# Performance work log

Measured on AMD Instinct MI355X. Metric: run time of the kernel, lower is better.

Reference implementation:

```python
import jax, jax.numpy as jnp
import numpy as np

EPS = 0.0  # torch code divides by norms directly (no eps); inputs are randn so norms > 0


def setup_inputs() -> dict:
    key = jax.random.key(0)
    ks = jax.random.split(key, 16)
    B, C, H, W = 16, 64, 128, 128
    DIM = 4 * C  # 256
    f32 = jnp.float32
    inp = {
        "low": jax.random.normal(ks[0], (B, C, H, W), f32),
        "high": jax.random.normal(ks[1], (B, C, H, W), f32),
        "flow": jax.random.normal(ks[2], (B, C, H, W), f32),
        "feedback": jax.random.normal(ks[3], (B, C, H, W), f32),
        # GCN(4, 64, 64): single graph-conv layer, relu(adj @ x @ W + b)
        "Wgcn": jax.random.normal(ks[4], (C, C), f32) * 0.05,
        "bgcn": jnp.zeros((C,), f32),
        # four SE fc heads: Linear(DIM -> C) + sigmoid
        "W1": jax.random.normal(ks[5], (C, DIM), f32) * 0.05,
        "b1": jnp.zeros((C,), f32),
        "W2": jax.random.normal(ks[6], (C, DIM), f32) * 0.05,
        "b2": jnp.zeros((C,), f32),
        "W3": jax.random.normal(ks[7], (C, DIM), f32) * 0.05,
        "b3": jnp.zeros((C,), f32),
        "W4": jax.random.normal(ks[8], (C, DIM), f32) * 0.05,
        "b4": jnp.zeros((C,), f32),
        # gate: 1x1 Conv2d(DIM -> 64) stored as dense [64, DIM]
        "Wgate": jax.random.normal(ks[9], (C, DIM), f32) * 0.05,
        "bgate": jnp.zeros((C,), f32),
    }
    return inp


def reference(low, high, flow, feedback, Wgcn, bgcn, W1, b1, W2, b2, W3, b3, W4, b4, Wgate, bgate):
    B, C, H, W = low.shape
    # adaptive avg pool(1) of concat([low,high,flow,feedback], dim=1) then view(B,4,C)
    combined_fc = jnp.stack([
        low.mean(axis=(2, 3)),
        high.mean(axis=(2, 3)),
        flow.mean(axis=(2, 3)),
        feedback.mean(axis=(2, 3)),
    ], axis=1)  # [B, 4, C]
    # cosine-similarity adjacency  [B, 4, 4]
    norm = jnp.linalg.norm(combined_fc, axis=2, keepdims=True)  # [B,4,1]
    mul = jnp.einsum('bic,bjc->bij', combined_fc, combined_fc)
    batch_adj = mul / (norm * norm.transpose(0, 2, 1))
    # tiny GCN: relu(adj @ x @ W + b)  -> feat_cat = flatten over nodes
    h = jax.nn.relu(jnp.einsum('bij,bjc,cd->bid', batch_adj, combined_fc, Wgcn) + bgcn)  # [B,4,C]
    feat_cat = h.reshape(B, 4 * C)  # [B, 256]
    sig = jax.nn.sigmoid
    e1 = sig(feat_cat @ W1.T + b1)[:, :, None, None]  # [B,C,1,1]
    e2 = sig(feat_cat @ W2.T + b2)[:, :, None, None]
    e3 = sig(feat_cat @ W3.T + b3)[:, :, None, None]
    e4 = sig(feat_cat @ W4.T + b4)[:, :, None, None]
    wa = low + e2 * high + e3 * flow + e4 * feedback
    wb = e1 * low + high + e3 * flow + e4 * feedback
    wc = e1 * low + e2 * high + flow + e4 * feedback
    wd = e1 * low + e2 * high + e3 * flow + feedback
    feat = jnp.concatenate([wa, wb, wc, wd], axis=1)  # [B, 4C, H, W]
    # 1x1 conv == channel GEMM
    out = jnp.einsum('bchw,oc->bohw', feat, Wgate) + bgate[None, :, None, None]
    return out
```

## Files before the change

### kernel.cpp

```cpp
#include <hip/hip_runtime.h>
#include <cmath>

#define BB 16
#define CC 64
#define PP 16384

typedef float f32x4 __attribute__((ext_vector_type(4)));

__global__ __launch_bounds__(256) void k_means(const float* __restrict__ low,
                                               const float* __restrict__ high,
                                               const float* __restrict__ flow,
                                               const float* __restrict__ fb,
                                               float* __restrict__ cf) {
    int blk = blockIdx.x;
    int b = blk >> 8, t = (blk >> 6) & 3, c = blk & 63;
    const float* in = (t == 0) ? low : (t == 1) ? high : (t == 2) ? flow : fb;
    const float4* p = (const float4*)(in + ((size_t)(b * CC + c)) * PP);
    int tid = threadIdx.x;

    float s = 0.f;
    #pragma unroll
    for (int i = 0; i < 16; ++i) {
        float4 v = p[tid + i * 256];
        s += (v.x + v.y) + (v.z + v.w);
    }
    #pragma unroll
    for (int off = 32; off > 0; off >>= 1) s += __shfl_down(s, off, 64);

    __shared__ float r[4];
    if ((tid & 63) == 0) r[tid >> 6] = s;
    __syncthreads();
    if (tid == 0)
        cf[(b * 4 + t) * CC + c] = ((r[0] + r[1]) + (r[2] + r[3])) * (1.0f / PP);
}

__global__ __launch_bounds__(256) void k_small(const float* __restrict__ cf,
    const float* __restrict__ Wgcn, const float* __restrict__ bgcn,
    const float* __restrict__ W1, const float* __restrict__ b1,
    const float* __restrict__ W2, const float* __restrict__ b2,
    const float* __restrict__ W3, const float* __restrict__ b3,
    const float* __restrict__ W4, const float* __restrict__ b4,
    const float* __restrict__ Wgate,
    float* __restrict__ Amat) {
    int b = blockIdx.x;
    int tid = threadIdx.x;
    int lane = tid & 63;
    int wid = tid >> 6;
    __shared__ float x[4][64];
    __shared__ float nrm[4];
    __shared__ float adj[16];
    __shared__ float y[4][64];
    __shared__ float fc[256];
    __shared__ float e[4][64];

    x[wid][lane] = cf[b * 256 + tid];
    __syncthreads();

    if (tid < 4) {
        float s = 0.f;
        for (int c = 0; c < 64; ++c) s += x[tid][c] * x[tid][c];
        nrm[tid] = sqrtf(s);
    }
    __syncthreads();

    if (tid < 16) {
        int i = tid >> 2, j = tid & 3;
        float s = 0.f;
        for (int c = 0; c < 64; ++c) s += x[i][c] * x[j][c];
        adj[tid] = s / (nrm[i] * nrm[j]);
    }
    __syncthreads();

    {
        float s = 0.f;
        #pragma unroll
        for (int j = 0; j < 4; ++j) s += adj[wid * 4 + j] * x[j][lane];
        y[wid][lane] = s;
    }
    __syncthreads();

    {
        float s = bgcn[lane];
        for (int c = 0; c < 64; ++c) s += y[wid][c] * Wgcn[c * 64 + lane];
        fc[wid * 64 + lane] = fmaxf(s, 0.f);
    }
    __syncthreads();

    {
        const float* Wk = (wid == 0) ? W1 : (wid == 1) ? W2 : (wid == 2) ? W3 : W4;
        const float* bk = (wid == 0) ? b1 : (wid == 1) ? b2 : (wid == 2) ? b3 : b4;
        float4 fv = *(const float4*)&fc[lane * 4];
        for (int c = 0; c < 64; ++c) {
            float4 w = *(const float4*)(Wk + c * 256 + lane * 4);
            float part = (w.x * fv.x + w.y * fv.y) + (w.z * fv.z + w.w * fv.w);
            #pragma unroll
            for (int off = 32; off > 0; off >>= 1)
                part += __shfl_down(part, off, 64);
            if (lane == 0) {
                float s = part + bk[c];
                e[wid][c] = 1.f / (1.f + expf(-s));
            }
        }
    }
    __syncthreads();

    {
        int t = wid, o = lane;
        const float* wrow = Wgate + o * 256;
        float* Ab = Amat + b * 16384 + t * 4096;
        #pragma unroll 4
        for (int c4 = 0; c4 < 64; c4 += 4) {
            float4 w0 = *(const float4*)(wrow + c4);
            float4 w1 = *(const float4*)(wrow + 64 + c4);
            float4 w2 = *(const float4*)(wrow + 128 + c4);
            float4 w3 = *(const float4*)(wrow + 192 + c4);
            float4 wt = (t == 0) ? w0 : (t == 1) ? w1 : (t == 2) ? w2 : w3;
            float4 sm = make_float4((w0.x + w1.x) + (w2.x + w3.x),
                                    (w0.y + w1.y) + (w2.y + w3.y),
                                    (w0.z + w1.z) + (w2.z + w3.z),
                                    (w0.w + w1.w) + (w2.w + w3.w));
            Ab[(c4 + 0) * 64 + o] = wt.x + e[t][c4 + 0] * (sm.x - wt.x);
            Ab[(c4 + 1) * 64 + o] = wt.y + e[t][c4 + 1] * (sm.y - wt.y);
            Ab[(c4 + 2) * 64 + o] = wt.z + e[t][c4 + 2] * (sm.z - wt.z);
            Ab[(c4 + 3) * 64 + o] = wt.w + e[t][c4 + 3] * (sm.w - wt.w);
        }
    }
}

__global__ __launch_bounds__(256, 4) void k_gemm(const float* __restrict__ low,
    const float* __restrict__ high, const float* __restrict__ flow,
    const float* __restrict__ fb, const float* __restrict__ Amat,
    const float* __restrict__ bgate, float* __restrict__ out) {
    int blk = blockIdx.x;
    int b = blk >> 6;
    int tile = blk & 63;
    int tid = threadIdx.x;
    int pt = tid & 63;
    int og = __builtin_amdgcn_readfirstlane(tid >> 6);
    int p0 = tile * 256 + pt * 4;

    size_t xoff = (size_t)b * (CC * PP) + p0;
    const float* pl = low  + xoff;
    const float* ph = high + xoff;
    const float* pf = flow + xoff;
    const float* pb = fb   + xoff;
    const float* Ab = Amat + b * 16384 + og * 16;

    float acc[16][4];
    #pragma unroll
    for (int j = 0; j < 16; ++j)
        #pragma unroll
        for (int q = 0; q < 4; ++q) acc[j][q] = 0.f;

    #pragma unroll 2
    for (int c = 0; c < 64; ++c) {
        float4 x0 = *(const float4*)(pl + (size_t)c * PP);
        float4 x1 = *(const float4*)(ph + (size_t)c * PP);
        float4 x2 = *(const float4*)(pf + (size_t)c * PP);
        float4 x3 = *(const float4*)(pb + (size_t)c * PP);
        const float* A0 = Ab + c * 64;
        #pragma unroll
        for (int j = 0; j < 16; ++j) {
            float a0 = A0[j];
            float a1 = A0[4096 + j];
            float a2 = A0[8192 + j];
            float a3 = A0[12288 + j];
            acc[j][0] += a0 * x0.x + a1 * x1.x + a2 * x2.x + a3 * x3.x;
            acc[j][1] += a0 * x0.y + a1 * x1.y + a2 * x2.y + a3 * x3.y;
            acc[j][2] += a0 * x0.z + a1 * x1.z + a2 * x2.z + a3 * x3.z;
            acc[j][3] += a0 * x0.w + a1 * x1.w + a2 * x2.w + a3 * x3.w;
        }
    }

    #pragma unroll
    for (int j = 0; j < 16; ++j) {
        int o = og * 16 + j;
        float bg = bgate[o];
        f32x4 r;
        r.x = acc[j][0] + bg; r.y = acc[j][1] + bg;
        r.z = acc[j][2] + bg; r.w = acc[j][3] + bg;
        __builtin_nontemporal_store(r, (f32x4*)(out + ((size_t)(b * CC + o)) * PP + p0));
    }
}

extern "C" void kernel_launch(void* const* d_in, const int* in_sizes, int n_in,
                              void* d_out, int out_size, void* d_ws, size_t ws_size,
                              hipStream_t stream) {
    const float* low  = (const float*)d_in[0];
    const float* high = (const float*)d_in[1];
    const float* flow = (const float*)d_in[2];
    const float* fb   = (const float*)d_in[3];
    const float* Wgcn = (const float*)d_in[4];
    const float* bgcn = (const float*)d_in[5];
    const float* W1   = (const float*)d_in[6];
    const float* b1   = (const float*)d_in[7];
    const float* W2   = (const float*)d_in[8];
    const float* b2   = (const float*)d_in[9];
    const float* W3   = (const float*)d_in[10];
    const float* b3   = (const float*)d_in[11];
    const float* W4   = (const float*)d_in[12];
    const float* b4   = (const float*)d_in[13];
    const float* Wgate = (const float*)d_in[14];
    const float* bgate = (const float*)d_in[15];
    float* out = (float*)d_out;

    float* cf   = (float*)d_ws;
    float* Amat = (float*)d_ws + 4096;

    k_means<<<BB * 4 * CC, 256, 0, stream>>>(low, high, flow, fb, cf);
    k_small<<<BB, 256, 0, stream>>>(cf, Wgcn, bgcn, W1, b1, W2, b2, W3, b3,
                                    W4, b4, Wgate, Amat);
    k_gemm<<<BB * CC, 256, 0, stream>>>(low, high, flow, fb, Amat, bgate, out);
}
```

Baseline: 450.5 us.

## Use packed FP32 FMA in gate GEMM and drop nontemporal stores

The inner GEMM loop is rewritten to accumulate pairs of output channels in 2-wide float vectors with elementwise FMA, so the compiler can emit packed FP32 FMA instructions and halve the scalar FMA count. The launch-bounds occupancy hint is lowered from 4 to 3 blocks per CU to leave more registers for the vectorized accumulators. Output stores become regular stores instead of nontemporal stores. Fewer resident waves and ordinary store caching may weaken memory latency hiding on this bandwidth-heavy kernel.

```diff
diff --git a/kernel.cpp b/kernel.cpp
--- a/kernel.cpp
+++ b/kernel.cpp
@@ -6,6 +6,7 @@
 #define PP 16384
 
 typedef float f32x4 __attribute__((ext_vector_type(4)));
+typedef float f32x2 __attribute__((ext_vector_type(2)));
 
 __global__ __launch_bounds__(256) void k_means(const float* __restrict__ low,
                                                const float* __restrict__ high,
@@ -127,7 +128,7 @@
     }
 }
 
-__global__ __launch_bounds__(256, 4) void k_gemm(const float* __restrict__ low,
+__global__ __launch_bounds__(256, 3) void k_gemm(const float* __restrict__ low,
     const float* __restrict__ high, const float* __restrict__ flow,
     const float* __restrict__ fb, const float* __restrict__ Amat,
     const float* __restrict__ bgate, float* __restrict__ out) {
@@ -140,46 +141,48 @@
     int p0 = tile * 256 + pt * 4;
 
     size_t xoff = (size_t)b * (CC * PP) + p0;
-    const float* pl = low  + xoff;
-    const float* ph = high + xoff;
-    const float* pf = flow + xoff;
-    const float* pb = fb   + xoff;
+    const float* px[4] = {low + xoff, high + xoff, flow + xoff, fb + xoff};
     const float* Ab = Amat + b * 16384 + og * 16;
 
-    float acc[16][4];
-    #pragma unroll
-    for (int j = 0; j < 16; ++j)
-        #pragma unroll
-        for (int q = 0; q < 4; ++q) acc[j][q] = 0.f;
+    f32x2 acc[8][4];
+    #pragma unroll
+    for (int j2 = 0; j2 < 8; ++j2)
+        #pragma unroll
+        for (int q = 0; q < 4; ++q) acc[j2][q] = (f32x2)(0.f);
 
     #pragma unroll 2
     for (int c = 0; c < 64; ++c) {
-        float4 x0 = *(const float4*)(pl + (size_t)c * PP);
-        float4 x1 = *(const float4*)(ph + (size_t)c * PP);
-        float4 x2 = *(const float4*)(pf + (size_t)c * PP);
-        float4 x3 = *(const float4*)(pb + (size_t)c * PP);
-        const float* A0 = Ab + c * 64;
-        #pragma unroll
-        for (int j = 0; j < 16; ++j) {
-            float a0 = A0[j];
-            float a1 = A0[4096 + j];
-            float a2 = A0[8192 + j];
-            float a3 = A0[12288 + j];
-            acc[j][0] += a0 * x0.x + a1 * x1.x + a2 * x2.x + a3 * x3.x;
-            acc[j][1] += a0 * x0.y + a1 * x1.y + a2 * x2.y + a3 * x3.y;
-            acc[j][2] += a0 * x0.z + a1 * x1.z + a2 * x2.z + a3 * x3.z;
-            acc[j][3] += a0 * x0.w + a1 * x1.w + a2 * x2.w + a3 * x3.w;
-        }
-    }
-
-    #pragma unroll
-    for (int j = 0; j < 16; ++j) {
-        int o = og * 16 + j;
-        float bg = bgate[o];
-        f32x4 r;
-        r.x = acc[j][0] + bg; r.y = acc[j][1] + bg;
-        r.z = acc[j][2] + bg; r.w = acc[j][3] + bg;
-        __builtin_nontemporal_store(r, (f32x4*)(out + ((size_t)(b * CC + o)) * PP + p0));
+        f32x4 xv[4];
+        #pragma unroll
+        for (int t = 0; t < 4; ++t)
+            xv[t] = *(const f32x4*)(px[t] + (size_t)c * PP);
+        #pragma unroll
+        for (int t = 0; t < 4; ++t) {
+            const f32x2* ap = (const f32x2*)(Ab + t * 4096 + c * 64);
+            #pragma unroll
+            for (int q = 0; q < 4; ++q) {
+                f32x2 xb;
+                xb.x = xv[t][q]; xb.y = xv[t][q];
+                #pragma unroll
+                for (int j2 = 0; j2 < 8; ++j2)
+                    acc[j2][q] = __builtin_elementwise_fma(ap[j2], xb, acc[j2][q]);
+            }
+        }
+    }
+
+    #pragma unroll
+    for (int j2 = 0; j2 < 8; ++j2) {
+        #pragma unroll
+        for (int par = 0; par < 2; ++par) {
+            int o = og * 16 + j2 * 2 + par;
+            float bg = bgate[o];
+            f32x4 r;
+            r.x = acc[j2][0][par] + bg;
+            r.y = acc[j2][1][par] + bg;
+            r.z = acc[j2][2][par] + bg;
+            r.w = acc[j2][3][par] + bg;
+            *(f32x4*)(out + ((size_t)(b * CC + o)) * PP + p0) = r;
+        }
     }
 }
 
```

After: 426.1 us. -5.4%, faster.
